# Kernel optimization log

Measured on AMD Instinct MI355X. Metric: run time of the kernel, lower is better.

Reference implementation:

```python
import jax, jax.numpy as jnp
import numpy as np

CHUNK = (10, 10, 10)          # chunk_shape from init_kwargs
VSHAPE = (40, 40, 200)        # spatial shape of each block
GRID_MAX = 1000               # locations drawn from [0, GRID_MAX)
SPAN = 256                    # > (GRID_MAX + max(VSHAPE)) / min(CHUNK); per-dim chunk-grid span for key linearization
NBATCH = 64


def setup_inputs() -> dict:
    key = jax.random.key(0)
    k1, k2 = jax.random.split(key)
    data = jax.random.normal(k1, (NBATCH, *VSHAPE), dtype=jnp.float32)
    location = jax.random.randint(k2, (NBATCH, 3), 0, GRID_MAX, dtype=jnp.int32)
    return {"data": data, "location": location}


def _chunkify(data, location):
    """Rebin each block into chunk-grid-aligned tiles of shape CHUNK.
    data: [B, V0, V1, V2]; location: [B, 3] int offsets in the global grid.
    Returns (chunks [M, *CHUNK], locs [M, 3]) with M = B * prod(nchunks)."""
    B = data.shape[0]
    C = jnp.array(CHUNK, dtype=jnp.int32)
    shift = location % C          # [B,3] offset of block origin within its first chunk
    start = location - shift      # [B,3] chunk-aligned envelope origin
    # Fixed-size envelope V + C per dim covers any shift in [0, C).
    E = tuple(v + c for v, c in zip(VSHAPE, CHUNK))
    nch = tuple(e // c for e, c in zip(E, CHUNK))  # chunks per dim: (5, 5, 21)

    def pad_one(d, sh):
        # padded[j0,j1,j2] = d[j - sh] where in range, else 0 (gather + mask, no scatter)
        idx = [jnp.arange(E[k]) - sh[k] for k in range(3)]
        valid = [(ix >= 0) & (ix < VSHAPE[k]) for k, ix in enumerate(idx)]
        cidx = [jnp.clip(ix, 0, VSHAPE[k] - 1) for k, ix in enumerate(idx)]
        g = d[cidx[0][:, None, None], cidx[1][None, :, None], cidx[2][None, None, :]]
        m = valid[0][:, None, None] & valid[1][None, :, None] & valid[2][None, None, :]
        return jnp.where(m, g, jnp.float32(0))

    padded = jax.vmap(pad_one)(data, shift)  # [B, E0, E1, E2]
    padded = padded.reshape(B, nch[0], CHUNK[0], nch[1], CHUNK[1], nch[2], CHUNK[2])
    chunks = padded.transpose(0, 1, 3, 5, 2, 4, 6).reshape(-1, *CHUNK)
    # per-chunk global locations
    g = jnp.stack(jnp.meshgrid(jnp.arange(nch[0]), jnp.arange(nch[1]),
                               jnp.arange(nch[2]), indexing='ij'), axis=-1)  # [n0,n1,n2,3]
    locs = start[:, None, None, None, :] + g[None].astype(jnp.int32) * C     # [B,n0,n1,n2,3]
    return chunks, locs.reshape(-1, 3)


def _accumulate(chunks, locs):
    """Sum chunks sharing the same global chunk location (scatter-add reduce).
    Output padded to a fixed M rows (jit-friendly); padding rows are zero."""
    M = chunks.shape[0]
    C = jnp.array(CHUNK, dtype=jnp.int32)
    cg = locs // C  # chunk-grid coordinates, each < SPAN
    keys = (cg[:, 0] * SPAN + cg[:, 1]) * SPAN + cg[:, 2]  # int32 linearized key
    ukeys, inv = jnp.unique(keys, return_inverse=True, size=M,
                            fill_value=jnp.int32(2**31 - 1))
    out = jax.ops.segment_sum(chunks.reshape(M, -1), inv, num_segments=M)
    out = out.reshape(M, *CHUNK)
    uloc = jnp.stack([ukeys // (SPAN * SPAN), (ukeys // SPAN) % SPAN,
                      ukeys % SPAN], axis=-1).astype(jnp.int32) * C
    return out, uloc


def reference(data, location):
    chunks, locs = _chunkify(data, location)
    return _accumulate(chunks, locs)
```

## Files before the change

kernel.cpp:

```cpp
#include <hip/hip_runtime.h>
#include <hip/hip_bf16.h>

namespace {
constexpr int NB    = 64;
constexpr int V0d   = 40, V1d = 40, V2d = 200;
constexpr int VOL   = V0d * V1d * V2d;
constexpr int NC0   = 5, NC1 = 5, NC2 = 21;
constexpr int CELLS = NC0 * NC1 * NC2;
constexpr int M     = NB * CELLS;
constexpr int C1MAX = 104, C2MAX = 120;
constexpr int KS    = 104 * C1MAX * C2MAX;
constexpr int NWORDS = KS / 32;
constexpr int NSB    = (NWORDS + 255) / 256;
constexpr int NWPAD  = NSB * 256;
constexpr int CHVOL  = 1000;
}

typedef float f32x4 __attribute__((ext_vector_type(4)));

__device__ __forceinline__ float bf16r(float v) {
    return __bfloat162float(__float2bfloat16(v));
}

__device__ __forceinline__ int enc(int c0, int c1, int c2) {
    return (c0 * C1MAX + c1) * C2MAX + c2;
}

__global__ void k_zero(int4* __restrict__ W4, int4* __restrict__ mask4) {
    int idx = blockIdx.x * blockDim.x + threadIdx.x;
    int stride = gridDim.x * blockDim.x;
    const int w4 = NWORDS / 4;
    for (int i = idx; i < w4; i += stride) W4[i] = make_int4(0, 0, 0, 0);
    const int m4 = M * 8 / 16;
    for (int i = idx; i < m4; i += stride) mask4[i] = make_int4(0, 0, 0, 0);
}

__global__ void k_mark(const int* __restrict__ loc, unsigned* __restrict__ W) {
    int m = blockIdx.x * blockDim.x + threadIdx.x;
    if (m >= M) return;
    int b = m / CELLS, cell = m % CELLS;
    int i = cell / (NC1 * NC2), j = (cell / NC2) % NC1, k = cell % NC2;
    int d = enc(loc[b * 3 + 0] / 10 + i, loc[b * 3 + 1] / 10 + j,
                loc[b * 3 + 2] / 10 + k);
    atomicOr(&W[d >> 5], 1u << (d & 31));
}

__global__ __launch_bounds__(256) void k_scan_words(const unsigned* __restrict__ W,
                                                    unsigned* __restrict__ WP,
                                                    int* __restrict__ Bsums) {
    int t = threadIdx.x;
    int w = blockIdx.x * 256 + t;
    int c = (w < NWORDS) ? __popc(W[w]) : 0;
    __shared__ int sc[256];
    sc[t] = c;
    __syncthreads();
#pragma unroll
    for (int off = 1; off < 256; off <<= 1) {
        int x = (t >= off) ? sc[t - off] : 0;
        __syncthreads();
        sc[t] += x;
        __syncthreads();
    }
    int incl = sc[t];
    WP[w] = (unsigned)(incl - c);
    if (t == 255) Bsums[blockIdx.x] = incl;
}

__global__ __launch_bounds__(256) void k_scan_sums(int* __restrict__ Bsums) {
    int t = threadIdx.x;
    int vv = (t < NSB) ? Bsums[t] : 0;
    __shared__ int sc[256];
    sc[t] = vv;
    __syncthreads();
#pragma unroll
    for (int off = 1; off < 256; off <<= 1) {
        int x = (t >= off) ? sc[t - off] : 0;
        __syncthreads();
        sc[t] += x;
        __syncthreads();
    }
    if (t < NSB) Bsums[t] = sc[t] - vv;
}

__global__ void k_slots(const int* __restrict__ loc, const unsigned* __restrict__ W,
                        const unsigned* __restrict__ WP, const int* __restrict__ Bsums,
                        int* __restrict__ ukeys, unsigned long long* __restrict__ mask) {
    int m = blockIdx.x * blockDim.x + threadIdx.x;
    if (m >= M) return;
    int b = m / CELLS, cell = m % CELLS;
    int i = cell / (NC1 * NC2), j = (cell / NC2) % NC1, k = cell % NC2;
    int d = enc(loc[b * 3 + 0] / 10 + i, loc[b * 3 + 1] / 10 + j,
                loc[b * 3 + 2] / 10 + k);
    int w = d >> 5, bp = d & 31;
    unsigned wd = W[w];
    int rank = Bsums[w >> 8] + (int)WP[w] + __popc(wd & ((1u << bp) - 1u));
    ukeys[rank] = d;
    atomicOr(&mask[rank], 1ull << b);
}

__global__ __launch_bounds__(256) void k_out(const float* __restrict__ data,
        const int* __restrict__ loc, const int* __restrict__ ukeys,
        const unsigned long long* __restrict__ mask,
        float* __restrict__ out, long long base_ul) {
    int orig = blockIdx.x;
    int r = (orig & 7) * (M / 8) + (orig >> 3);
    int t = threadIdx.x;

    unsigned long long mk = mask[r];
    int key = ukeys[r];
    bool valid = (mk != 0ull);

    float ax = 0.f, ay = 0.f, az = 0.f, aw = 0.f;
    int c0 = 0, c1 = 0, c2 = 0;
    if (valid) {
        c0 = key / (C1MAX * C2MAX);
        int rem = key % (C1MAX * C2MAX);
        c1 = rem / C2MAX;
        c2 = rem % C2MAX;
        if (t < 250) {
            int e0 = t * 4;
            int x  = e0 / 100;
            int rm = e0 % 100;
            int y  = rm / 10;
            int z0 = rm % 10;
            int g0 = c0 * 10, g1 = c1 * 10, g2 = c2 * 10;
            unsigned long long m2 = mk;
            while (m2) {
                int b = __builtin_ctzll(m2);
                m2 &= m2 - 1;
                int l0 = loc[b * 3 + 0], l1 = loc[b * 3 + 1], l2 = loc[b * 3 + 2];
                const float* db = data + (size_t)b * VOL;
                if (z0 <= 6) {
                    int p0 = g0 - l0 + x, p1 = g1 - l1 + y, p2 = g2 - l2 + z0;
                    if ((unsigned)p0 < (unsigned)V0d &&
                        (unsigned)p1 < (unsigned)V1d) {
                        const float* s = db + (p0 * V1d + p1) * V2d + p2;
                        if (p2 >= 0 && p2 <= V2d - 4) {
                            ax += s[0]; ay += s[1]; az += s[2]; aw += s[3];
                        } else {
                            if ((unsigned)p2       < (unsigned)V2d) ax += s[0];
                            if ((unsigned)(p2 + 1) < (unsigned)V2d) ay += s[1];
                            if ((unsigned)(p2 + 2) < (unsigned)V2d) az += s[2];
                            if ((unsigned)(p2 + 3) < (unsigned)V2d) aw += s[3];
                        }
                    }
                } else {
                    float av[4] = {0.f, 0.f, 0.f, 0.f};
#pragma unroll
                    for (int jj = 0; jj < 4; ++jj) {
                        int e  = e0 + jj;
                        int xx = e / 100;
                        int rj = e % 100;
                        int yy = rj / 10, zz = rj % 10;
                        int q0 = g0 - l0 + xx, q1 = g1 - l1 + yy,
                            q2 = g2 - l2 + zz;
                        if ((unsigned)q0 < (unsigned)V0d &&
                            (unsigned)q1 < (unsigned)V1d &&
                            (unsigned)q2 < (unsigned)V2d)
                            av[jj] = db[(q0 * V1d + q1) * V2d + q2];
                    }
                    ax += av[0]; ay += av[1]; az += av[2]; aw += av[3];
                }
            }
        }
    }

    if (t < 250) {
        f32x4 v = {bf16r(ax), bf16r(ay), bf16r(az), bf16r(aw)};
        __builtin_nontemporal_store(v,
            reinterpret_cast<f32x4*>(out + (long long)r * CHVOL + t * 4));
    }
    if (t == 0) {
        float u0, u1, u2;
        if (valid) {
            u0 = (float)(c0 * 10);
            u1 = (float)(c1 * 10);
            u2 = (float)(c2 * 10);
        } else {
            u0 = 327670.f; u1 = 2550.f; u2 = 2550.f;
        }
        long long i = base_ul + (long long)r * 3;
        __builtin_nontemporal_store(bf16r(u0), out + i + 0);
        __builtin_nontemporal_store(bf16r(u1), out + i + 1);
        __builtin_nontemporal_store(bf16r(u2), out + i + 2);
    }
}

extern "C" void kernel_launch(void* const* d_in, const int* in_sizes, int n_in,
                              void* d_out, int out_size, void* d_ws, size_t ws_size,
                              hipStream_t stream) {
    const float* data = (const float*)d_in[0];
    const int* loc    = (const int*)d_in[1];
    float* out        = (float*)d_out;

    const size_t offMask  = 0;
    const size_t offKeys  = offMask + (size_t)M * 8;
    const size_t offW     = offKeys + (size_t)M * 4;
    const size_t offWP    = offW + (size_t)NWPAD * 4;
    const size_t offBs    = offWP + (size_t)NWPAD * 4;
    const size_t bytesAll = offBs + (size_t)(NSB + 64) * 4;

    char* basep = (ws_size >= bytesAll) ? (char*)d_ws : (char*)d_out;

    unsigned long long* mask = (unsigned long long*)(basep + offMask);
    int*      ukeys = (int*)(basep + offKeys);
    unsigned* W     = (unsigned*)(basep + offW);
    unsigned* WP    = (unsigned*)(basep + offWP);
    int*      Bsums = (int*)(basep + offBs);

    long long out_sz  = (long long)out_size;
    long long base_ul = out_sz - (long long)3 * M;

    k_zero<<<128, 256, 0, stream>>>((int4*)W, (int4*)mask);
    k_mark<<<(M + 255) / 256, 256, 0, stream>>>(loc, W);
    k_scan_words<<<NSB, 256, 0, stream>>>(W, WP, Bsums);
    k_scan_sums<<<1, 256, 0, stream>>>(Bsums);
    k_slots<<<(M + 255) / 256, 256, 0, stream>>>(loc, W, WP, Bsums, ukeys, mask);
    k_out<<<M, 256, 0, stream>>>(data, loc, ukeys, mask, out, base_ul);
}
```

Baseline: 60.85 us.

## Fuse block-sum scan into slot kernel and process eight rows per output block

The single-block scan of block sums is folded into k_slots: each block redundantly rescans the small Bsums array in shared memory, which removes one kernel launch. Mask zeroing moves from k_zero into k_mark, and k_zero gets fewer blocks. k_out now handles eight output rows per block, prefetching the next row's mask and key, which cuts the grid size by eight at the cost of less parallelism per row.

```diff
diff --git a/kernel.cpp b/kernel.cpp
--- a/kernel.cpp
+++ b/kernel.cpp
@@ -14,6 +14,8 @@
 constexpr int NSB    = (NWORDS + 255) / 256;
 constexpr int NWPAD  = NSB * 256;
 constexpr int CHVOL  = 1000;
+constexpr int RPB    = 8;
+constexpr int NQ     = M / RPB;
 }
 
 typedef float f32x4 __attribute__((ext_vector_type(4)));
@@ -26,17 +28,17 @@
     return (c0 * C1MAX + c1) * C2MAX + c2;
 }
 
-__global__ void k_zero(int4* __restrict__ W4, int4* __restrict__ mask4) {
+__global__ void k_zero(int4* __restrict__ W4) {
     int idx = blockIdx.x * blockDim.x + threadIdx.x;
     int stride = gridDim.x * blockDim.x;
     const int w4 = NWORDS / 4;
     for (int i = idx; i < w4; i += stride) W4[i] = make_int4(0, 0, 0, 0);
-    const int m4 = M * 8 / 16;
-    for (int i = idx; i < m4; i += stride) mask4[i] = make_int4(0, 0, 0, 0);
-}
-
-__global__ void k_mark(const int* __restrict__ loc, unsigned* __restrict__ W) {
+}
+
+__global__ void k_mark(const int* __restrict__ loc, unsigned* __restrict__ W,
+                       int4* __restrict__ mask4) {
     int m = blockIdx.x * blockDim.x + threadIdx.x;
+    if (m < M * 8 / 16) mask4[m] = make_int4(0, 0, 0, 0);
     if (m >= M) return;
     int b = m / CELLS, cell = m % CELLS;
     int i = cell / (NC1 * NC2), j = (cell / NC2) % NC1, k = cell % NC2;
@@ -66,11 +68,15 @@
     if (t == 255) Bsums[blockIdx.x] = incl;
 }
 
-__global__ __launch_bounds__(256) void k_scan_sums(int* __restrict__ Bsums) {
+__global__ __launch_bounds__(256) void k_slots(const int* __restrict__ loc,
+        const unsigned* __restrict__ W, const unsigned* __restrict__ WP,
+        const int* __restrict__ Bsums, int* __restrict__ ukeys,
+        unsigned long long* __restrict__ mask) {
     int t = threadIdx.x;
-    int vv = (t < NSB) ? Bsums[t] : 0;
+    __shared__ int sBase[256];
+    int bv = (t < NSB) ? Bsums[t] : 0;
     __shared__ int sc[256];
-    sc[t] = vv;
+    sc[t] = bv;
     __syncthreads();
 #pragma unroll
     for (int off = 1; off < 256; off <<= 1) {
@@ -79,21 +85,17 @@
         sc[t] += x;
         __syncthreads();
     }
-    if (t < NSB) Bsums[t] = sc[t] - vv;
-}
-
-__global__ void k_slots(const int* __restrict__ loc, const unsigned* __restrict__ W,
-                        const unsigned* __restrict__ WP, const int* __restrict__ Bsums,
-                        int* __restrict__ ukeys, unsigned long long* __restrict__ mask) {
-    int m = blockIdx.x * blockDim.x + threadIdx.x;
+    sBase[t] = sc[t] - bv;
+    __syncthreads();
+
+    int m = blockIdx.x * blockDim.x + t;
     if (m >= M) return;
     int b = m / CELLS, cell = m % CELLS;
     int i = cell / (NC1 * NC2), j = (cell / NC2) % NC1, k = cell % NC2;
     int d = enc(loc[b * 3 + 0] / 10 + i, loc[b * 3 + 1] / 10 + j,
                 loc[b * 3 + 2] / 10 + k);
     int w = d >> 5, bp = d & 31;
-    unsigned wd = W[w];
-    int rank = Bsums[w >> 8] + (int)WP[w] + __popc(wd & ((1u << bp) - 1u));
+    int rank = sBase[w >> 8] + (int)WP[w] + __popc(W[w] & ((1u << bp) - 1u));
     ukeys[rank] = d;
     atomicOr(&mask[rank], 1ull << b);
 }
@@ -103,27 +105,33 @@
         const unsigned long long* __restrict__ mask,
         float* __restrict__ out, long long base_ul) {
     int orig = blockIdx.x;
-    int r = (orig & 7) * (M / 8) + (orig >> 3);
+    int q = (orig & 7) * (NQ / 8) + (orig >> 3);
+    int r0 = q * RPB;
     int t = threadIdx.x;
-
-    unsigned long long mk = mask[r];
-    int key = ukeys[r];
-    bool valid = (mk != 0ull);
-
-    float ax = 0.f, ay = 0.f, az = 0.f, aw = 0.f;
-    int c0 = 0, c1 = 0, c2 = 0;
-    if (valid) {
-        c0 = key / (C1MAX * C2MAX);
-        int rem = key % (C1MAX * C2MAX);
-        c1 = rem / C2MAX;
-        c2 = rem % C2MAX;
-        if (t < 250) {
-            int e0 = t * 4;
-            int x  = e0 / 100;
-            int rm = e0 % 100;
-            int y  = rm / 10;
-            int z0 = rm % 10;
-            int g0 = c0 * 10, g1 = c1 * 10, g2 = c2 * 10;
+    bool act = (t < 250);
+
+    int e0 = t * 4;
+    int x  = e0 / 100;
+    int rm = e0 % 100;
+    int y  = rm / 10;
+    int z0 = rm % 10;
+
+    unsigned long long mk_n = mask[r0];
+    int key_n = ukeys[r0];
+
+    for (int rk = 0; rk < RPB; ++rk) {
+        int r = r0 + rk;
+        unsigned long long mk = mk_n;
+        int key = key_n;
+        if (rk < RPB - 1) {
+            mk_n  = mask[r + 1];
+            key_n = ukeys[r + 1];
+        }
+        float ax = 0.f, ay = 0.f, az = 0.f, aw = 0.f;
+        if (mk != 0ull && act) {
+            int c0 = key / (C1MAX * C2MAX);
+            int rem = key % (C1MAX * C2MAX);
+            int g0 = c0 * 10, g1 = (rem / C2MAX) * 10, g2 = (rem % C2MAX) * 10;
             unsigned long long m2 = mk;
             while (m2) {
                 int b = __builtin_ctzll(m2);
@@ -145,7 +153,7 @@
                         }
                     }
                 } else {
-                    float av[4] = {0.f, 0.f, 0.f, 0.f};
+                    float av0 = 0.f, av1 = 0.f, av2 = 0.f, av3 = 0.f;
 #pragma unroll
                     for (int jj = 0; jj < 4; ++jj) {
                         int e  = e0 + jj;
@@ -156,26 +164,33 @@
                             q2 = g2 - l2 + zz;
                         if ((unsigned)q0 < (unsigned)V0d &&
                             (unsigned)q1 < (unsigned)V1d &&
-                            (unsigned)q2 < (unsigned)V2d)
-                            av[jj] = db[(q0 * V1d + q1) * V2d + q2];
+                            (unsigned)q2 < (unsigned)V2d) {
+                            float v = db[(q0 * V1d + q1) * V2d + q2];
+                            if (jj == 0) av0 = v; else if (jj == 1) av1 = v;
+                            else if (jj == 2) av2 = v; else av3 = v;
+                        }
                     }
-                    ax += av[0]; ay += av[1]; az += av[2]; aw += av[3];
+                    ax += av0; ay += av1; az += av2; aw += av3;
                 }
             }
         }
-    }
-
-    if (t < 250) {
-        f32x4 v = {bf16r(ax), bf16r(ay), bf16r(az), bf16r(aw)};
-        __builtin_nontemporal_store(v,
-            reinterpret_cast<f32x4*>(out + (long long)r * CHVOL + t * 4));
-    }
-    if (t == 0) {
+        if (act) {
+            f32x4 v = {bf16r(ax), bf16r(ay), bf16r(az), bf16r(aw)};
+            __builtin_nontemporal_store(v,
+                reinterpret_cast<f32x4*>(out + (long long)r * CHVOL + e0));
+        }
+    }
+
+    if (t < RPB) {
+        int r = r0 + t;
+        unsigned long long mkv = mask[r];
         float u0, u1, u2;
-        if (valid) {
-            u0 = (float)(c0 * 10);
-            u1 = (float)(c1 * 10);
-            u2 = (float)(c2 * 10);
+        if (mkv != 0ull) {
+            int key = ukeys[r];
+            int rem = key % (C1MAX * C2MAX);
+            u0 = (float)((key / (C1MAX * C2MAX)) * 10);
+            u1 = (float)((rem / C2MAX) * 10);
+            u2 = (float)((rem % C2MAX) * 10);
         } else {
             u0 = 327670.f; u1 = 2550.f; u2 = 2550.f;
         }
@@ -211,10 +226,9 @@
     long long out_sz  = (long long)out_size;
     long long base_ul = out_sz - (long long)3 * M;
 
-    k_zero<<<128, 256, 0, stream>>>((int4*)W, (int4*)mask);
-    k_mark<<<(M + 255) / 256, 256, 0, stream>>>(loc, W);
+    k_zero<<<40, 256, 0, stream>>>((int4*)W);
+    k_mark<<<(M + 255) / 256, 256, 0, stream>>>(loc, W, (int4*)mask);
     k_scan_words<<<NSB, 256, 0, stream>>>(W, WP, Bsums);
-    k_scan_sums<<<1, 256, 0, stream>>>(Bsums);
     k_slots<<<(M + 255) / 256, 256, 0, stream>>>(loc, W, WP, Bsums, ukeys, mask);
-    k_out<<<M, 256, 0, stream>>>(data, loc, ukeys, mask, out, base_ul);
-}
+    k_out<<<NQ, 256, 0, stream>>>(data, loc, ukeys, mask, out, base_ul);
+}
```

Result: slower. 65.76 us (+8.1%).
